# Kernel tuning notes

Hardware: AMD Instinct MI355X
Metric: run time of the kernel (lower is better)

Reference implementation:

```python
import jax, jax.numpy as jnp
import numpy as np

N = 100000      # num nodes
E = 600000      # num edges
DIN = 64        # input_dim
DH = 128        # hidden_dim
G = 512         # num graphs
EPS = 1e-5      # BatchNorm eps


def setup_inputs() -> dict:
    key = jax.random.key(0)
    ks = jax.random.split(key, 12)
    x = jax.random.normal(ks[0], (N, DIN), jnp.float32)
    edge_index = jax.random.randint(ks[1], (2, E), 0, N)
    batch = jnp.sort(jax.random.randint(ks[2], (N,), 0, G))

    def w(k, shape):
        return (jax.random.normal(k, shape, jnp.float32) / np.float32(np.sqrt(shape[0])))

    inp = {"x": x, "edge_index": edge_index, "batch": batch}
    inp.update(
        W1=w(ks[3], (DIN, DH)), b1=jnp.zeros((DH,), jnp.float32),
        bn1_g=jnp.ones((DH,), jnp.float32), bn1_b=jnp.zeros((DH,), jnp.float32),
        bn1_m=jax.random.normal(ks[4], (DH,), jnp.float32) * 0.1,
        bn1_v=jnp.ones((DH,), jnp.float32),
        W2=w(ks[5], (DH, DH)), b2=jnp.zeros((DH,), jnp.float32),
        bn2_g=jnp.ones((DH,), jnp.float32), bn2_b=jnp.zeros((DH,), jnp.float32),
        bn2_m=jax.random.normal(ks[6], (DH,), jnp.float32) * 0.1,
        bn2_v=jnp.ones((DH,), jnp.float32),
        W3=w(ks[7], (DH, DH)), b3=jnp.zeros((DH,), jnp.float32),
        bn3_g=jnp.ones((DH,), jnp.float32), bn3_b=jnp.zeros((DH,), jnp.float32),
        bn3_m=jax.random.normal(ks[8], (DH,), jnp.float32) * 0.1,
        bn3_v=jnp.ones((DH,), jnp.float32),
        fc1_w=w(ks[9], (DH, DH // 2)), fc1_b=jnp.zeros((DH // 2,), jnp.float32),
        fc2_w=w(ks[10], (DH // 2, 1)), fc2_b=jnp.zeros((1,), jnp.float32),
    )
    return inp


def reference(x, edge_index, batch,
              W1, b1, bn1_g, bn1_b, bn1_m, bn1_v,
              W2, b2, bn2_g, bn2_b, bn2_m, bn2_v,
              W3, b3, bn3_g, bn3_b, bn3_m, bn3_v,
              fc1_w, fc1_b, fc2_w, fc2_b):
    # --- GCN normalization with self-loops (PyG GCNConv, sym norm) ---
    loop = jnp.arange(N, dtype=edge_index.dtype)
    src = jnp.concatenate([edge_index[0], loop])  # [E+N]
    dst = jnp.concatenate([edge_index[1], loop])  # [E+N]
    deg = jax.ops.segment_sum(jnp.ones_like(dst, jnp.float32), dst, num_segments=N)
    dis = jnp.where(deg > 0, jax.lax.rsqrt(jnp.maximum(deg, 1.0)), 0.0)
    norm = (dis[src] * dis[dst])[:, None]  # [E+N, 1]

    def conv(h, W, b):
        h = h @ W
        agg = jax.ops.segment_sum(h[src] * norm, dst, num_segments=N)
        return agg + b

    def bn(h, g, bta, m, v):
        return (h - m) * jax.lax.rsqrt(v + EPS) * g + bta  # eval-mode BatchNorm1d

    # block 1 (dropout is identity in eval)
    h = jax.nn.relu(bn(conv(x, W1, b1), bn1_g, bn1_b, bn1_m, bn1_v))
    # middle residual block (num_layers=3 -> one block)
    h = jax.nn.relu(bn(conv(h, W2, b2), bn2_g, bn2_b, bn2_m, bn2_v)) + h
    # output conv block
    h = jax.nn.relu(bn(conv(h, W3, b3), bn3_g, bn3_b, bn3_m, bn3_v))

    # global mean pool over graphs
    sums = jax.ops.segment_sum(h, batch, num_segments=G)          # [G, DH]
    cnt = jax.ops.segment_sum(jnp.ones((N, 1), h.dtype), batch, num_segments=G)
    pooled = sums / jnp.maximum(cnt, 1.0)

    h = jax.nn.relu(pooled @ fc1_w + fc1_b)
    return jax.nn.sigmoid(h @ fc2_w + fc2_b)  # [G, 1]
```

## Files before the change

kernel.cpp:

```cpp
#include <hip/hip_runtime.h>
#include <math.h>

#define N_NODES 100000
#define N_EDGES 600000
#define DIN     64
#define DH      128
#define NG      512
#define EPS_BN  1e-5f
#define SCAN_TPB 256
#define N_SCAN_BLK ((N_NODES + SCAN_TPB - 1) / SCAN_TPB)

typedef unsigned short u16;
typedef short s16x8 __attribute__((ext_vector_type(8)));
typedef float f32x4 __attribute__((ext_vector_type(4)));

__device__ __forceinline__ u16 f2bf(float x) {
    unsigned u = __builtin_bit_cast(unsigned, x);
    u += 0x7fffu + ((u >> 16) & 1u);
    return (u16)(u >> 16);
}
__device__ __forceinline__ float bf2f(u16 h) {
    unsigned u = ((unsigned)h) << 16;
    return __builtin_bit_cast(float, u);
}

__global__ __launch_bounds__(256) void deg_kernel(const int* __restrict__ dst,
                                                  float* __restrict__ deg, int E) {
    int e = blockIdx.x * blockDim.x + threadIdx.x;
    if (e < E) atomicAdd(&deg[dst[e]], 1.0f);
}

__global__ __launch_bounds__(256) void dis_kernel(const float* __restrict__ deg,
                                                  float* __restrict__ dis,
                                                  int* __restrict__ deg_i, int n) {
    int i = blockIdx.x * blockDim.x + threadIdx.x;
    if (i < n) {
        float d = deg[i];
        dis[i] = rsqrtf(d + 1.0f);
        deg_i[i] = (int)d;
    }
}

__global__ __launch_bounds__(SCAN_TPB) void scan1_kernel(const int* __restrict__ deg_i,
                                                         int* __restrict__ row_ptr,
                                                         int* __restrict__ blk, int n) {
    __shared__ int sm[SCAN_TPB];
    const int t = threadIdx.x;
    const int i = blockIdx.x * SCAN_TPB + t;
    const int v = (i < n) ? deg_i[i] : 0;
    sm[t] = v;
    __syncthreads();
#pragma unroll
    for (int off = 1; off < SCAN_TPB; off <<= 1) {
        int u = (t >= off) ? sm[t - off] : 0;
        __syncthreads();
        sm[t] += u;
        __syncthreads();
    }
    if (i < n) row_ptr[i] = sm[t] - v;
    if (t == SCAN_TPB - 1) blk[blockIdx.x] = sm[t];
}

__global__ __launch_bounds__(512) void scan2_kernel(int* __restrict__ blk,
                                                    int* __restrict__ row_ptr,
                                                    int nblk, int n) {
    __shared__ int sm[512];
    const int t = threadIdx.x;
    const int v = (t < nblk) ? blk[t] : 0;
    sm[t] = v;
    __syncthreads();
#pragma unroll
    for (int off = 1; off < 512; off <<= 1) {
        int u = (t >= off) ? sm[t - off] : 0;
        __syncthreads();
        sm[t] += u;
        __syncthreads();
    }
    if (t < nblk) blk[t] = sm[t] - v;
    if (t == nblk - 1) row_ptr[n] = sm[t];
}

__global__ __launch_bounds__(SCAN_TPB) void scan3_kernel(int* __restrict__ row_ptr,
                                                         const int* __restrict__ blk, int n) {
    const int i = blockIdx.x * SCAN_TPB + threadIdx.x;
    if (i < n) row_ptr[i] += blk[blockIdx.x];
}

__global__ __launch_bounds__(256) void build_csr_kernel(const int* __restrict__ src,
                                                        const int* __restrict__ dst,
                                                        const float* __restrict__ dis,
                                                        const int* __restrict__ row_ptr,
                                                        int* __restrict__ cursor,
                                                        int* __restrict__ col,
                                                        float* __restrict__ val, int E) {
    int e = blockIdx.x * blockDim.x + threadIdx.x;
    if (e >= E) return;
    const int s = src[e];
    const int d = dst[e];
    const int p = atomicAdd(&cursor[d], 1);
    const int idx = row_ptr[d] + p;
    col[idx] = s;
    val[idx] = dis[s] * dis[d];
}

__global__ __launch_bounds__(256) void xcvt_kernel(const float* __restrict__ x,
                                                   u16* __restrict__ xb, long n) {
    long i = ((long)blockIdx.x * blockDim.x + threadIdx.x) * 8;
    if (i >= n) return;
    const float4 a = *(const float4*)(x + i);
    const float4 b = *(const float4*)(x + i + 4);
    s16x8 o;
    o[0] = (short)f2bf(a.x); o[1] = (short)f2bf(a.y);
    o[2] = (short)f2bf(a.z); o[3] = (short)f2bf(a.w);
    o[4] = (short)f2bf(b.x); o[5] = (short)f2bf(b.y);
    o[6] = (short)f2bf(b.z); o[7] = (short)f2bf(b.w);
    *(s16x8*)(xb + i) = o;
}

__global__ __launch_bounds__(256) void wt_kernel(const float* __restrict__ W,
                                                 u16* __restrict__ Wt, int K, int N) {
    int idx = blockIdx.x * blockDim.x + threadIdx.x;
    if (idx >= K * N) return;
    int k = idx / N, n = idx % N;
    Wt[(long)n * K + k] = f2bf(W[idx]);
}

__global__ __launch_bounds__(256) void bn_prep_kernel(
    const float* b1, const float* g1, const float* bb1, const float* m1, const float* v1,
    const float* b2, const float* g2, const float* bb2, const float* m2, const float* v2,
    const float* b3, const float* g3, const float* bb3, const float* m3, const float* v3,
    float* __restrict__ sc, float* __restrict__ sh) {
    int i = blockIdx.x * blockDim.x + threadIdx.x;
    if (i >= 3 * DH) return;
    int l = i >> 7, c = i & (DH - 1);
    const float* bc = l == 0 ? b1 : (l == 1 ? b2 : b3);
    const float* g  = l == 0 ? g1 : (l == 1 ? g2 : g3);
    const float* bb = l == 0 ? bb1 : (l == 1 ? bb2 : bb3);
    const float* m  = l == 0 ? m1 : (l == 1 ? m2 : m3);
    const float* v  = l == 0 ? v1 : (l == 1 ? v2 : v3);
    float s = g[c] * rsqrtf(v[c] + EPS_BN);
    sc[i] = s;
    sh[i] = (bc[c] - m[c]) * s + bb[c];
}

template <int K>
__global__ __launch_bounds__(256) void gemm_mfma(const u16* __restrict__ A,
                                                 const u16* __restrict__ Wt,
                                                 u16* __restrict__ C,
                                                 int M) {
    const int wave = threadIdx.x >> 6;
    const int lane = threadIdx.x & 63;
    const int r16 = lane & 15;
    const int kc  = lane >> 4;
    const long row0 = (long)blockIdx.x * 64 + wave * 16;

    f32x4 acc[8];
#pragma unroll
    for (int t = 0; t < 8; ++t)
#pragma unroll
        for (int q = 0; q < 4; ++q) acc[t][q] = 0.0f;

    long arow = row0 + r16;
    if (arow >= M) arow = M - 1;
    const u16* ap = A + arow * K + kc * 8;

#pragma unroll
    for (int ks = 0; ks < K; ks += 32) {
        const s16x8 a = *(const s16x8*)(ap + ks);
#pragma unroll
        for (int t = 0; t < 8; ++t) {
            const s16x8 b = *(const s16x8*)(Wt + (long)(t * 16 + r16) * K + ks + kc * 8);
            acc[t] = __builtin_amdgcn_mfma_f32_16x16x32_bf16(a, b, acc[t], 0, 0, 0);
        }
    }

#pragma unroll
    for (int r = 0; r < 4; ++r) {
        const long row = row0 + kc * 4 + r;
        if (row < M) {
            u16* cp = C + row * DH + r16;
#pragma unroll
            for (int t = 0; t < 8; ++t) cp[t * 16] = f2bf(acc[t][r]);
        }
    }
}

template <bool RES>
__global__ __launch_bounds__(256) void agg_epi_kernel(const u16* __restrict__ H,
                                                      const int* __restrict__ row_ptr,
                                                      const int* __restrict__ col,
                                                      const float* __restrict__ val,
                                                      const float* __restrict__ dis,
                                                      const float* __restrict__ scl,
                                                      const float* __restrict__ shf,
                                                      u16* __restrict__ out, int n) {
    const long t = (long)blockIdx.x * blockDim.x + threadIdx.x;
    const int lane = (int)(t & 15);
    const long i = t >> 4;
    if (i >= n) return;
    const int c = lane * 8;

    float d2 = dis[i];
    d2 *= d2;
    float acc[8];
    const s16x8 hv = *(const s16x8*)(H + i * DH + c);
#pragma unroll
    for (int q = 0; q < 8; ++q) acc[q] = bf2f((u16)hv[q]) * d2;

    const int beg = row_ptr[i];
    const int end = row_ptr[i + 1];
    for (int e = beg; e < end; ++e) {
        const int s = col[e];
        const float nm = val[e];
        const s16x8 v = *(const s16x8*)(H + (long)s * DH + c);
#pragma unroll
        for (int q = 0; q < 8; ++q) acc[q] = fmaf(bf2f((u16)v[q]), nm, acc[q]);
    }

    const float4 s0 = *(const float4*)(scl + c);
    const float4 s1 = *(const float4*)(scl + c + 4);
    const float4 f0 = *(const float4*)(shf + c);
    const float4 f1 = *(const float4*)(shf + c + 4);
    const float sv[8] = {s0.x, s0.y, s0.z, s0.w, s1.x, s1.y, s1.z, s1.w};
    const float fv[8] = {f0.x, f0.y, f0.z, f0.w, f1.x, f1.y, f1.z, f1.w};

    float r[8];
#pragma unroll
    for (int q = 0; q < 8; ++q) r[q] = fmaxf(fmaf(acc[q], sv[q], fv[q]), 0.0f);
    if (RES) {
        const s16x8 rv = *(const s16x8*)(out + i * DH + c);
#pragma unroll
        for (int q = 0; q < 8; ++q) r[q] += bf2f((u16)rv[q]);
    }
    s16x8 ov;
#pragma unroll
    for (int q = 0; q < 8; ++q) ov[q] = (short)f2bf(r[q]);
    *(s16x8*)(out + i * DH + c) = ov;
}

__global__ __launch_bounds__(256) void graph_bounds_kernel(const int* __restrict__ batch,
                                                           int* __restrict__ gp) {
    int g = blockIdx.x * blockDim.x + threadIdx.x;
    if (g > NG) return;
    int lo = 0, hi = N_NODES;
    while (lo < hi) {
        int mid = (lo + hi) >> 1;
        if (batch[mid] < g) lo = mid + 1; else hi = mid;
    }
    gp[g] = lo;
}

__global__ __launch_bounds__(256) void pool_kernel(const u16* __restrict__ h,
                                                   const int* __restrict__ gp,
                                                   float* __restrict__ pooled) {
    const int g = blockIdx.x;
    const int t = threadIdx.x;
    const int grp = t >> 4;
    const int cl = t & 15;
    const int c = cl * 8;
    const int beg = gp[g];
    const int end = gp[g + 1];

    float acc[8] = {0, 0, 0, 0, 0, 0, 0, 0};
    for (int i = beg + grp; i < end; i += 16) {
        const s16x8 v = *(const s16x8*)(h + (long)i * DH + c);
#pragma unroll
        for (int q = 0; q < 8; ++q) acc[q] += bf2f((u16)v[q]);
    }

    __shared__ float sm[16][DH];
#pragma unroll
    for (int q = 0; q < 8; ++q) sm[grp][c + q] = acc[q];
    __syncthreads();

    if (t < DH) {
        float s = 0.0f;
#pragma unroll
        for (int r = 0; r < 16; ++r) s += sm[r][t];
        pooled[(long)g * DH + t] = s / fmaxf((float)(end - beg), 1.0f);
    }
}

__global__ __launch_bounds__(64) void head_kernel(const float* __restrict__ pooled,
                                                  const float* __restrict__ fc1w,
                                                  const float* __restrict__ fc1b,
                                                  const float* __restrict__ fc2w,
                                                  const float* __restrict__ fc2b,
                                                  float* __restrict__ out) {
    const int g = blockIdx.x;
    const int j = threadIdx.x;
    __shared__ float p[DH];
    p[j]      = pooled[(long)g * DH + j];
    p[j + 64] = pooled[(long)g * DH + 64 + j];
    __syncthreads();

    float acc = 0.0f;
#pragma unroll 4
    for (int k = 0; k < DH; ++k) acc = fmaf(p[k], fc1w[(long)k * 64 + j], acc);
    const float h1 = fmaxf(acc + fc1b[j], 0.0f);
    float v = h1 * fc2w[j];
#pragma unroll
    for (int off = 32; off > 0; off >>= 1) v += __shfl_down(v, off);
    if (j == 0) out[g] = 1.0f / (1.0f + expf(-(v + fc2b[0])));
}

extern "C" void kernel_launch(void* const* d_in, const int* in_sizes, int n_in,
                              void* d_out, int out_size, void* d_ws, size_t ws_size,
                              hipStream_t stream) {
    const float* x     = (const float*)d_in[0];
    const int*   ei    = (const int*)d_in[1];
    const int*   batch = (const int*)d_in[2];
    const float* W1 = (const float*)d_in[3];
    const float* b1 = (const float*)d_in[4];
    const float* g1 = (const float*)d_in[5];
    const float* t1 = (const float*)d_in[6];
    const float* m1 = (const float*)d_in[7];
    const float* v1 = (const float*)d_in[8];
    const float* W2 = (const float*)d_in[9];
    const float* b2 = (const float*)d_in[10];
    const float* g2 = (const float*)d_in[11];
    const float* t2 = (const float*)d_in[12];
    const float* m2 = (const float*)d_in[13];
    const float* v2 = (const float*)d_in[14];
    const float* W3 = (const float*)d_in[15];
    const float* b3 = (const float*)d_in[16];
    const float* g3 = (const float*)d_in[17];
    const float* t3 = (const float*)d_in[18];
    const float* m3 = (const float*)d_in[19];
    const float* v3 = (const float*)d_in[20];
    const float* fc1w = (const float*)d_in[21];
    const float* fc1b = (const float*)d_in[22];
    const float* fc2w = (const float*)d_in[23];
    const float* fc2b = (const float*)d_in[24];

    const int* src = ei;
    const int* dst = ei + N_EDGES;

    char* ws = (char*)d_ws;
    size_t off = 0;
    auto alloc = [&](size_t bytes) -> char* {
        char* p = ws + off;
        off = (off + bytes + 511) & ~(size_t)511;
        return p;
    };
    float* deg     = (float*)alloc((size_t)N_NODES * 4);
    float* dis     = (float*)alloc((size_t)N_NODES * 4);
    int*   deg_i   = (int*)  alloc((size_t)N_NODES * 4);
    int*   row_ptr = (int*)  alloc(((size_t)N_NODES + 1) * 4);
    int*   cursor  = (int*)  alloc((size_t)N_NODES * 4);
    int*   blk     = (int*)  alloc((size_t)N_SCAN_BLK * 4);
    int*   col     = (int*)  alloc((size_t)N_EDGES * 4);
    float* val     = (float*)alloc((size_t)N_EDGES * 4);
    int*   gp      = (int*)  alloc((size_t)(NG + 1) * 4);
    float* pooled  = (float*)alloc((size_t)NG * DH * 4);
    float* bnsc    = (float*)alloc((size_t)3 * DH * 4);
    float* bnsh    = (float*)alloc((size_t)3 * DH * 4);
    u16*   xb      = (u16*)  alloc((size_t)N_NODES * DIN * 2);
    u16*   Wt1     = (u16*)  alloc((size_t)DH * DIN * 2);
    u16*   Wt2     = (u16*)  alloc((size_t)DH * DH * 2);
    u16*   Wt3     = (u16*)  alloc((size_t)DH * DH * 2);
    u16*   bufB    = (u16*)  alloc((size_t)N_NODES * DH * 2);
    u16*   bufA    = (u16*)  alloc((size_t)N_NODES * DH * 2);

    const int TPB = 256;
    const int gEdge  = (N_EDGES + TPB - 1) / TPB;
    const int gNode  = (N_NODES + TPB - 1) / TPB;
    const int gGemm  = (N_NODES + 63) / 64;
    const int gAgg   = (int)(((long)N_NODES * 16 + TPB - 1) / TPB);

    hipMemsetAsync(deg, 0, (size_t)N_NODES * 4, stream);
    hipMemsetAsync(cursor, 0, (size_t)N_NODES * 4, stream);
    deg_kernel<<<gEdge, TPB, 0, stream>>>(dst, deg, N_EDGES);
    dis_kernel<<<gNode, TPB, 0, stream>>>(deg, dis, deg_i, N_NODES);
    scan1_kernel<<<N_SCAN_BLK, SCAN_TPB, 0, stream>>>(deg_i, row_ptr, blk, N_NODES);
    scan2_kernel<<<1, 512, 0, stream>>>(blk, row_ptr, N_SCAN_BLK, N_NODES);
    scan3_kernel<<<N_SCAN_BLK, SCAN_TPB, 0, stream>>>(row_ptr, blk, N_NODES);
    build_csr_kernel<<<gEdge, TPB, 0, stream>>>(src, dst, dis, row_ptr, cursor, col, val,
                                                N_EDGES);
    graph_bounds_kernel<<<3, 256, 0, stream>>>(batch, gp);

    xcvt_kernel<<<(int)(((long)N_NODES * DIN / 8 + TPB - 1) / TPB), TPB, 0, stream>>>(
        x, xb, (long)N_NODES * DIN);
    wt_kernel<<<(DIN * DH + TPB - 1) / TPB, TPB, 0, stream>>>(W1, Wt1, DIN, DH);
    wt_kernel<<<(DH * DH + TPB - 1) / TPB, TPB, 0, stream>>>(W2, Wt2, DH, DH);
    wt_kernel<<<(DH * DH + TPB - 1) / TPB, TPB, 0, stream>>>(W3, Wt3, DH, DH);
    bn_prep_kernel<<<2, TPB, 0, stream>>>(b1, g1, t1, m1, v1, b2, g2, t2, m2, v2,
                                          b3, g3, t3, m3, v3, bnsc, bnsh);

    gemm_mfma<DIN><<<gGemm, TPB, 0, stream>>>(xb, Wt1, bufB, N_NODES);
    agg_epi_kernel<false><<<gAgg, TPB, 0, stream>>>(bufB, row_ptr, col, val, dis,
                                                    bnsc, bnsh, bufA, N_NODES);
    gemm_mfma<DH><<<gGemm, TPB, 0, stream>>>(bufA, Wt2, bufB, N_NODES);
    agg_epi_kernel<true><<<gAgg, TPB, 0, stream>>>(bufB, row_ptr, col, val, dis,
                                                   bnsc + DH, bnsh + DH, bufA, N_NODES);
    gemm_mfma<DH><<<gGemm, TPB, 0, stream>>>(bufA, Wt3, bufB, N_NODES);
    agg_epi_kernel<false><<<gAgg, TPB, 0, stream>>>(bufB, row_ptr, col, val, dis,
                                                    bnsc + 2 * DH, bnsh + 2 * DH, bufA,
                                                    N_NODES);

    pool_kernel<<<NG, TPB, 0, stream>>>(bufA, gp, pooled);
    head_kernel<<<NG, 64, 0, stream>>>(pooled, fc1w, fc1b, fc2w, fc2b, (float*)d_out);
}
```

Before: 319.6 us.

## Fuse aggregation and GEMM per layer by aggregating before the weight multiply

Reorders each GCN layer to aggregate neighbour features first (A·H) and then apply W via MFMA from LDS, fusing aggregation, GEMM and BN/ReLU/residual epilogue into one kernel. This removes the intermediate HW buffer round trip and halves the number of layer kernel launches; layer 1 now gathers 64-wide inputs instead of 128-wide. CSR column and norm values are packed into one 64-bit array, and the two memsets are merged. The fused kernel has less parallelism during the gather phase (each 16-thread group handles 4 rows serially) and uses LDS, which may reduce occupancy.

```diff
diff --git a/kernel.cpp b/kernel.cpp
--- a/kernel.cpp
+++ b/kernel.cpp
@@ -11,7 +11,9 @@
 #define N_SCAN_BLK ((N_NODES + SCAN_TPB - 1) / SCAN_TPB)
 
 typedef unsigned short u16;
+typedef unsigned long long u64;
 typedef short s16x8 __attribute__((ext_vector_type(8)));
+typedef short s16x4 __attribute__((ext_vector_type(4)));
 typedef float f32x4 __attribute__((ext_vector_type(4)));
 
 __device__ __forceinline__ u16 f2bf(float x) {
@@ -91,16 +93,14 @@
                                                         const float* __restrict__ dis,
                                                         const int* __restrict__ row_ptr,
                                                         int* __restrict__ cursor,
-                                                        int* __restrict__ col,
-                                                        float* __restrict__ val, int E) {
+                                                        u64* __restrict__ colval, int E) {
     int e = blockIdx.x * blockDim.x + threadIdx.x;
     if (e >= E) return;
     const int s = src[e];
     const int d = dst[e];
     const int p = atomicAdd(&cursor[d], 1);
-    const int idx = row_ptr[d] + p;
-    col[idx] = s;
-    val[idx] = dis[s] * dis[d];
+    const unsigned fb = __builtin_bit_cast(unsigned, dis[s] * dis[d]);
+    colval[row_ptr[d] + p] = ((u64)fb << 32) | (unsigned)s;
 }
 
 __global__ __launch_bounds__(256) void xcvt_kernel(const float* __restrict__ x,
@@ -143,99 +143,119 @@
     sh[i] = (bc[c] - m[c]) * s + bb[c];
 }
 
-template <int K>
-__global__ __launch_bounds__(256) void gemm_mfma(const u16* __restrict__ A,
-                                                 const u16* __restrict__ Wt,
-                                                 u16* __restrict__ C,
-                                                 int M) {
-    const int wave = threadIdx.x >> 6;
-    const int lane = threadIdx.x & 63;
+template <int K, bool RES>
+__global__ __launch_bounds__(256) void layer_kernel(const u16* __restrict__ H,
+                                                    const u16* __restrict__ Hres,
+                                                    const u64* __restrict__ colval,
+                                                    const int* __restrict__ row_ptr,
+                                                    const float* __restrict__ dis,
+                                                    const u16* __restrict__ Wt,
+                                                    const float* __restrict__ scl,
+                                                    const float* __restrict__ shf,
+                                                    u16* __restrict__ out, int n) {
+    constexpr int EL = K / 16;
+    __shared__ u16 lds_a[64 * K];
+
+    const int tid = threadIdx.x;
+    const int g   = tid >> 4;
+    const int cl  = tid & 15;
+    const long base = (long)blockIdx.x * 64;
+
+    for (int rr = 0; rr < 4; ++rr) {
+        const int r_loc = g * 4 + rr;
+        const long i = base + r_loc;
+        float acc[EL];
+#pragma unroll
+        for (int q = 0; q < EL; ++q) acc[q] = 0.0f;
+        if (i < n) {
+            float d2 = dis[i];
+            d2 *= d2;
+            if constexpr (EL == 8) {
+                const s16x8 hv = *(const s16x8*)(H + i * K + cl * 8);
+#pragma unroll
+                for (int q = 0; q < 8; ++q) acc[q] = bf2f((u16)hv[q]) * d2;
+            } else {
+                const s16x4 hv = *(const s16x4*)(H + i * K + cl * 4);
+#pragma unroll
+                for (int q = 0; q < 4; ++q) acc[q] = bf2f((u16)hv[q]) * d2;
+            }
+            const int beg = row_ptr[i];
+            const int end = row_ptr[i + 1];
+            for (int e = beg; e < end; ++e) {
+                const u64 cv = colval[e];
+                const int s = (int)(unsigned)cv;
+                const float nm = __builtin_bit_cast(float, (unsigned)(cv >> 32));
+                if constexpr (EL == 8) {
+                    const s16x8 v = *(const s16x8*)(H + (long)s * K + cl * 8);
+#pragma unroll
+                    for (int q = 0; q < 8; ++q) acc[q] = fmaf(bf2f((u16)v[q]), nm, acc[q]);
+                } else {
+                    const s16x4 v = *(const s16x4*)(H + (long)s * K + cl * 4);
+#pragma unroll
+                    for (int q = 0; q < 4; ++q) acc[q] = fmaf(bf2f((u16)v[q]), nm, acc[q]);
+                }
+            }
+        }
+        if constexpr (EL == 8) {
+            const int cs = cl ^ (r_loc & 7);
+            s16x8 ov;
+#pragma unroll
+            for (int q = 0; q < 8; ++q) ov[q] = (short)f2bf(acc[q]);
+            *(s16x8*)&lds_a[r_loc * K + cs * 8] = ov;
+        } else {
+            const int cs = (cl >> 1) ^ (r_loc & 7);
+            s16x4 ov;
+#pragma unroll
+            for (int q = 0; q < 4; ++q) ov[q] = (short)f2bf(acc[q]);
+            *(s16x4*)&lds_a[r_loc * K + cs * 8 + (cl & 1) * 4] = ov;
+        }
+    }
+    __syncthreads();
+
+    const int wave = tid >> 6;
+    const int lane = tid & 63;
     const int r16 = lane & 15;
     const int kc  = lane >> 4;
-    const long row0 = (long)blockIdx.x * 64 + wave * 16;
-
-    f32x4 acc[8];
+    const int rl  = wave * 16 + r16;
+
+    f32x4 acc2[8];
 #pragma unroll
     for (int t = 0; t < 8; ++t)
 #pragma unroll
-        for (int q = 0; q < 4; ++q) acc[t][q] = 0.0f;
-
-    long arow = row0 + r16;
-    if (arow >= M) arow = M - 1;
-    const u16* ap = A + arow * K + kc * 8;
-
-#pragma unroll
-    for (int ks = 0; ks < K; ks += 32) {
-        const s16x8 a = *(const s16x8*)(ap + ks);
+        for (int q = 0; q < 4; ++q) acc2[t][q] = 0.0f;
+
+#pragma unroll
+    for (int ks = 0; ks < K / 32; ++ks) {
+        const int cs = (kc + ks * 4) ^ (rl & 7);
+        const s16x8 a = *(const s16x8*)&lds_a[rl * K + cs * 8];
 #pragma unroll
         for (int t = 0; t < 8; ++t) {
-            const s16x8 b = *(const s16x8*)(Wt + (long)(t * 16 + r16) * K + ks + kc * 8);
-            acc[t] = __builtin_amdgcn_mfma_f32_16x16x32_bf16(a, b, acc[t], 0, 0, 0);
+            const s16x8 b = *(const s16x8*)(Wt + (long)(t * 16 + r16) * K + ks * 32 + kc * 8);
+            acc2[t] = __builtin_amdgcn_mfma_f32_16x16x32_bf16(a, b, acc2[t], 0, 0, 0);
         }
     }
 
-#pragma unroll
-    for (int r = 0; r < 4; ++r) {
-        const long row = row0 + kc * 4 + r;
-        if (row < M) {
-            u16* cp = C + row * DH + r16;
-#pragma unroll
-            for (int t = 0; t < 8; ++t) cp[t * 16] = f2bf(acc[t][r]);
+    float scv[8], shv[8];
+#pragma unroll
+    for (int t = 0; t < 8; ++t) {
+        scv[t] = scl[t * 16 + r16];
+        shv[t] = shf[t * 16 + r16];
+    }
+
+#pragma unroll
+    for (int q = 0; q < 4; ++q) {
+        const long row = base + wave * 16 + kc * 4 + q;
+        if (row < n) {
+            u16* op = out + row * DH + r16;
+            const u16* rp = Hres + row * DH + r16;
+#pragma unroll
+            for (int t = 0; t < 8; ++t) {
+                float y = fmaxf(fmaf(acc2[t][q], scv[t], shv[t]), 0.0f);
+                if (RES) y += bf2f(rp[t * 16]);
+                op[t * 16] = f2bf(y);
+            }
         }
     }
-}
-
-template <bool RES>
-__global__ __launch_bounds__(256) void agg_epi_kernel(const u16* __restrict__ H,
-                                                      const int* __restrict__ row_ptr,
-                                                      const int* __restrict__ col,
-                                                      const float* __restrict__ val,
-                                                      const float* __restrict__ dis,
-                                                      const float* __restrict__ scl,
-                                                      const float* __restrict__ shf,
-                                                      u16* __restrict__ out, int n) {
-    const long t = (long)blockIdx.x * blockDim.x + threadIdx.x;
-    const int lane = (int)(t & 15);
-    const long i = t >> 4;
-    if (i >= n) return;
-    const int c = lane * 8;
-
-    float d2 = dis[i];
-    d2 *= d2;
-    float acc[8];
-    const s16x8 hv = *(const s16x8*)(H + i * DH + c);
-#pragma unroll
-    for (int q = 0; q < 8; ++q) acc[q] = bf2f((u16)hv[q]) * d2;
-
-    const int beg = row_ptr[i];
-    const int end = row_ptr[i + 1];
-    for (int e = beg; e < end; ++e) {
-        const int s = col[e];
-        const float nm = val[e];
-        const s16x8 v = *(const s16x8*)(H + (long)s * DH + c);
-#pragma unroll
-        for (int q = 0; q < 8; ++q) acc[q] = fmaf(bf2f((u16)v[q]), nm, acc[q]);
-    }
-
-    const float4 s0 = *(const float4*)(scl + c);
-    const float4 s1 = *(const float4*)(scl + c + 4);
-    const float4 f0 = *(const float4*)(shf + c);
-    const float4 f1 = *(const float4*)(shf + c + 4);
-    const float sv[8] = {s0.x, s0.y, s0.z, s0.w, s1.x, s1.y, s1.z, s1.w};
-    const float fv[8] = {f0.x, f0.y, f0.z, f0.w, f1.x, f1.y, f1.z, f1.w};
-
-    float r[8];
-#pragma unroll
-    for (int q = 0; q < 8; ++q) r[q] = fmaxf(fmaf(acc[q], sv[q], fv[q]), 0.0f);
-    if (RES) {
-        const s16x8 rv = *(const s16x8*)(out + i * DH + c);
-#pragma unroll
-        for (int q = 0; q < 8; ++q) r[q] += bf2f((u16)rv[q]);
-    }
-    s16x8 ov;
-#pragma unroll
-    for (int q = 0; q < 8; ++q) ov[q] = (short)f2bf(r[q]);
-    *(s16x8*)(out + i * DH + c) = ov;
 }
 
 __global__ __launch_bounds__(256) void graph_bounds_kernel(const int* __restrict__ batch,
@@ -343,14 +363,13 @@
         off = (off + bytes + 511) & ~(size_t)511;
         return p;
     };
-    float* deg     = (float*)alloc((size_t)N_NODES * 4);
+    float* deg     = (float*)alloc((size_t)2 * N_NODES * 4);
+    int*   cursor  = (int*)(deg + N_NODES);
     float* dis     = (float*)alloc((size_t)N_NODES * 4);
     int*   deg_i   = (int*)  alloc((size_t)N_NODES * 4);
     int*   row_ptr = (int*)  alloc(((size_t)N_NODES + 1) * 4);
-    int*   cursor  = (int*)  alloc((size_t)N_NODES * 4);
     int*   blk     = (int*)  alloc((size_t)N_SCAN_BLK * 4);
-    int*   col     = (int*)  alloc((size_t)N_EDGES * 4);
-    float* val     = (float*)alloc((size_t)N_EDGES * 4);
+    u64*   colval  = (u64*)  alloc((size_t)N_EDGES * 8);
     int*   gp      = (int*)  alloc((size_t)(NG + 1) * 4);
     float* pooled  = (float*)alloc((size_t)NG * DH * 4);
     float* bnsc    = (float*)alloc((size_t)3 * DH * 4);
@@ -359,23 +378,21 @@
     u16*   Wt1     = (u16*)  alloc((size_t)DH * DIN * 2);
     u16*   Wt2     = (u16*)  alloc((size_t)DH * DH * 2);
     u16*   Wt3     = (u16*)  alloc((size_t)DH * DH * 2);
-    u16*   bufB    = (u16*)  alloc((size_t)N_NODES * DH * 2);
-    u16*   bufA    = (u16*)  alloc((size_t)N_NODES * DH * 2);
+    u16*   buf1    = (u16*)  alloc((size_t)N_NODES * DH * 2);
+    u16*   buf2    = (u16*)  alloc((size_t)N_NODES * DH * 2);
 
     const int TPB = 256;
     const int gEdge  = (N_EDGES + TPB - 1) / TPB;
     const int gNode  = (N_NODES + TPB - 1) / TPB;
-    const int gGemm  = (N_NODES + 63) / 64;
-    const int gAgg   = (int)(((long)N_NODES * 16 + TPB - 1) / TPB);
-
-    hipMemsetAsync(deg, 0, (size_t)N_NODES * 4, stream);
-    hipMemsetAsync(cursor, 0, (size_t)N_NODES * 4, stream);
+    const int gLayer = (N_NODES + 63) / 64;
+
+    hipMemsetAsync(deg, 0, (size_t)2 * N_NODES * 4, stream);
     deg_kernel<<<gEdge, TPB, 0, stream>>>(dst, deg, N_EDGES);
     dis_kernel<<<gNode, TPB, 0, stream>>>(deg, dis, deg_i, N_NODES);
     scan1_kernel<<<N_SCAN_BLK, SCAN_TPB, 0, stream>>>(deg_i, row_ptr, blk, N_NODES);
     scan2_kernel<<<1, 512, 0, stream>>>(blk, row_ptr, N_SCAN_BLK, N_NODES);
     scan3_kernel<<<N_SCAN_BLK, SCAN_TPB, 0, stream>>>(row_ptr, blk, N_NODES);
-    build_csr_kernel<<<gEdge, TPB, 0, stream>>>(src, dst, dis, row_ptr, cursor, col, val,
+    build_csr_kernel<<<gEdge, TPB, 0, stream>>>(src, dst, dis, row_ptr, cursor, colval,
                                                 N_EDGES);
     graph_bounds_kernel<<<3, 256, 0, stream>>>(batch, gp);
 
@@ -387,17 +404,15 @@
     bn_prep_kernel<<<2, TPB, 0, stream>>>(b1, g1, t1, m1, v1, b2, g2, t2, m2, v2,
                                           b3, g3, t3, m3, v3, bnsc, bnsh);
 
-    gemm_mfma<DIN><<<gGemm, TPB, 0, stream>>>(xb, Wt1, bufB, N_NODES);
-    agg_epi_kernel<false><<<gAgg, TPB, 0, stream>>>(bufB, row_ptr, col, val, dis,
-                                                    bnsc, bnsh, bufA, N_NODES);
-    gemm_mfma<DH><<<gGemm, TPB, 0, stream>>>(bufA, Wt2, bufB, N_NODES);
-    agg_epi_kernel<true><<<gAgg, TPB, 0, stream>>>(bufB, row_ptr, col, val, dis,
-                                                   bnsc + DH, bnsh + DH, bufA, N_NODES);
-    gemm_mfma<DH><<<gGemm, TPB, 0, stream>>>(bufA, Wt3, bufB, N_NODES);
-    agg_epi_kernel<false><<<gAgg, TPB, 0, stream>>>(bufB, row_ptr, col, val, dis,
-                                                    bnsc + 2 * DH, bnsh + 2 * DH, bufA,
-                                                    N_NODES);
-
-    pool_kernel<<<NG, TPB, 0, stream>>>(bufA, gp, pooled);
+    layer_kernel<DIN, false><<<gLayer, TPB, 0, stream>>>(xb, xb, colval, row_ptr, dis,
+                                                         Wt1, bnsc, bnsh, buf1, N_NODES);
+    layer_kernel<DH, true><<<gLayer, TPB, 0, stream>>>(buf1, buf1, colval, row_ptr, dis,
+                                                       Wt2, bnsc + DH, bnsh + DH, buf2,
+                                                       N_NODES);
+    layer_kernel<DH, false><<<gLayer, TPB, 0, stream>>>(buf2, buf2, colval, row_ptr, dis,
+                                                        Wt3, bnsc + 2 * DH, bnsh + 2 * DH,
+                                                        buf1, N_NODES);
+
+    pool_kernel<<<NG, TPB, 0, stream>>>(buf1, gp, pooled);
     head_kernel<<<NG, 64, 0, stream>>>(pooled, fc1w, fc1b, fc2w, fc2b, (float*)d_out);
 }
```

Result: slower. 349.6 us (+9.4%).
